# Performance work log

Hardware: AMD Instinct MI355X
Metric: run time of the kernel (lower is better)

## Reference

```python
import jax, jax.numpy as jnp
import numpy as np

D_MODEL = 1024
NUM_HEADS = 16
D_K = D_MODEL // NUM_HEADS
THETA = 10000.0
SEQ = 4096
BATCH = 1


def _rope(x, pos):
    # x: [..., S, d_k]; pos: [S]
    inv_freq = 1.0 / (THETA ** (jnp.arange(0, D_K, 2, dtype=jnp.float32) / D_K))  # [d_k/2]
    freqs = pos.astype(jnp.float32)[:, None] * inv_freq[None, :]  # [S, d_k/2]
    cos = jnp.cos(freqs)
    sin = jnp.sin(freqs)
    x_even = x[..., ::2]
    x_odd = x[..., 1::2]
    out1 = cos * x_even - sin * x_odd
    out2 = sin * x_even + cos * x_odd
    # interleave: stack on new last axis then flatten (matches torch.stack(...,-1).flatten(-2))
    out = jnp.stack([out1, out2], axis=-1).reshape(x.shape)
    return out


def setup_inputs() -> dict:
    key = jax.random.key(0)
    ks = jax.random.split(key, 5)
    std = (2.0 / (D_MODEL + D_MODEL)) ** 0.5
    x = jax.random.normal(ks[0], (BATCH, SEQ, D_MODEL), dtype=jnp.float32)
    wq = jax.random.normal(ks[1], (D_MODEL, D_MODEL), dtype=jnp.float32) * std
    wk = jax.random.normal(ks[2], (D_MODEL, D_MODEL), dtype=jnp.float32) * std
    wv = jax.random.normal(ks[3], (D_MODEL, D_MODEL), dtype=jnp.float32) * std
    wo = jax.random.normal(ks[4], (D_MODEL, D_MODEL), dtype=jnp.float32) * std
    return {"x": x, "wq": wq, "wk": wk, "wv": wv, "wo": wo}


def reference(x, wq, wk, wv, wo):
    b, s, d = x.shape
    # projections: y = x @ W.T  (weight stored [out, in])
    q = jnp.einsum('bsd,od->bso', x, wq)
    k = jnp.einsum('bsd,od->bso', x, wk)
    v = jnp.einsum('bsd,od->bso', x, wv)
    # split heads -> [b, h, s, d_k]
    q = q.reshape(b, s, NUM_HEADS, D_K).transpose(0, 2, 1, 3)
    k = k.reshape(b, s, NUM_HEADS, D_K).transpose(0, 2, 1, 3)
    v = v.reshape(b, s, NUM_HEADS, D_K).transpose(0, 2, 1, 3)
    pos = jnp.arange(s)
    q = _rope(q, pos)
    k = _rope(k, pos)
    scores = jnp.einsum('bhqd,bhkd->bhqk', q, k) / (D_K ** 0.5)
    causal = jnp.tril(jnp.ones((s, s), dtype=bool))
    scores = jnp.where(causal, scores, -jnp.inf)
    attn = jax.nn.softmax(scores, axis=-1)
    out = jnp.einsum('bhqk,bhkd->bhqd', attn, v)
    out = out.transpose(0, 2, 1, 3).reshape(b, s, d)
    out = jnp.einsum('bsd,od->bso', out, wo)
    return out
```

## Files before the change

kernel.cpp:

```cpp
#include <hip/hip_runtime.h>
#include <math.h>

#define SEQ    4096
#define DMODEL 1024
#define NHEADS 16
#define DK     64

typedef unsigned short u16;
typedef short bh8 __attribute__((ext_vector_type(8)));
typedef float f4  __attribute__((ext_vector_type(4)));
typedef float f16v __attribute__((ext_vector_type(16)));

__device__ __forceinline__ u16 f2b(float f) {
    union { float f; unsigned u; } v; v.f = f;
    unsigned u = v.u;
    return (u16)((u + 0x7FFFu + ((u >> 16) & 1u)) >> 16);
}
__device__ __forceinline__ unsigned pk2(float a, float b) {
    union { float f; unsigned u; } ua, ub; ua.f = a; ub.f = b;
    return (ua.u >> 16) | (ub.u & 0xFFFF0000u);
}

__global__ void cvt_all_kernel(const float* __restrict__ x,
                               const float* __restrict__ wq, const float* __restrict__ wk,
                               const float* __restrict__ wv, const float* __restrict__ wo,
                               u16* __restrict__ xb, u16* __restrict__ wb)
{
    const int NX = SEQ * DMODEL / 8;
    const int NW = DMODEL * DMODEL / 8;
    int i = blockIdx.x * blockDim.x + threadIdx.x;
    if (i >= NX + 4 * NW) return;
    const float* src; u16* dst; int j;
    if (i < NX) { src = x; dst = xb; j = i; }
    else {
        int k = i - NX;
        int wsel = k >> 17;
        j = k & (NW - 1);
        src = (wsel == 0) ? wq : (wsel == 1) ? wk : (wsel == 2) ? wv : wo;
        dst = wb + (size_t)wsel * DMODEL * DMODEL;
    }
    const float4* p = (const float4*)src + (size_t)j * 2;
    float4 a = p[0], b = p[1];
    __align__(16) u16 r[8] = { f2b(a.x), f2b(a.y), f2b(a.z), f2b(a.w),
                               f2b(b.x), f2b(b.y), f2b(b.z), f2b(b.w) };
    *(uint4*)(dst + (size_t)j * 8) = *(const uint4*)r;
}

template<int MODE>
__global__ __launch_bounds__(256) void gemm_bt(
    const u16* __restrict__ A, const u16* __restrict__ B,
    void* __restrict__ out, u16* __restrict__ Qh, u16* __restrict__ Kh,
    u16* __restrict__ Vt, int M, int N, int K)
{
    constexpr int BN = (MODE == 0) ? 64 : 128;
    constexpr int NJ = BN / 32;

    __shared__ __align__(16) u16 As[128 * 32];
    __shared__ __align__(16) u16 Bs[BN * 32];

    const int t    = threadIdx.x;
    const int w    = t >> 6, lane = t & 63;
    const int quad = lane >> 4, l16 = lane & 15;
    const int wm   = w >> 1,  wn  = w & 1;
    const int m0   = blockIdx.y * 128, n0 = blockIdx.x * BN;
    const int lr   = lane >> 2;
    const int lc   = (lane & 3) * 8;

    f4 acc[4][NJ];
#pragma unroll
    for (int i = 0; i < 4; ++i)
#pragma unroll
        for (int j = 0; j < NJ; ++j) { f4 z = {0.f,0.f,0.f,0.f}; acc[i][j] = z; }

    const int c0 = 2 * w, c1 = 2 * w + 1;

    for (int k0 = 0; k0 < K; k0 += 32) {
        __builtin_amdgcn_global_load_lds(
            (const __attribute__((address_space(1))) unsigned int*)(A + (size_t)(m0 + c0*16 + lr)*K + k0 + lc),
            (__attribute__((address_space(3))) unsigned int*)(As + c0*512), 16, 0, 0);
        __builtin_amdgcn_global_load_lds(
            (const __attribute__((address_space(1))) unsigned int*)(A + (size_t)(m0 + c1*16 + lr)*K + k0 + lc),
            (__attribute__((address_space(3))) unsigned int*)(As + c1*512), 16, 0, 0);
        if (MODE == 0) {
            __builtin_amdgcn_global_load_lds(
                (const __attribute__((address_space(1))) unsigned int*)(B + (size_t)(n0 + w*16 + lr)*K + k0 + lc),
                (__attribute__((address_space(3))) unsigned int*)(Bs + w*512), 16, 0, 0);
        } else {
            __builtin_amdgcn_global_load_lds(
                (const __attribute__((address_space(1))) unsigned int*)(B + (size_t)(n0 + c0*16 + lr)*K + k0 + lc),
                (__attribute__((address_space(3))) unsigned int*)(Bs + c0*512), 16, 0, 0);
            __builtin_amdgcn_global_load_lds(
                (const __attribute__((address_space(1))) unsigned int*)(B + (size_t)(n0 + c1*16 + lr)*K + k0 + lc),
                (__attribute__((address_space(3))) unsigned int*)(Bs + c1*512), 16, 0, 0);
        }
        __syncthreads();

        bh8 af[4], bf_[NJ];
#pragma unroll
        for (int i = 0; i < 4; ++i)
            af[i] = *(const bh8*)&As[(wm*64 + i*16 + l16)*32 + quad*8];
#pragma unroll
        for (int j = 0; j < NJ; ++j)
            bf_[j] = *(const bh8*)&Bs[(wn*(BN/2) + j*16 + l16)*32 + quad*8];
#pragma unroll
        for (int i = 0; i < 4; ++i)
#pragma unroll
            for (int j = 0; j < NJ; ++j)
                acc[i][j] = __builtin_amdgcn_mfma_f32_16x16x32_bf16(af[i], bf_[j], acc[i][j], 0, 0, 0);
        __syncthreads();
    }

    if (MODE == 0) {
#pragma unroll
        for (int i = 0; i < 4; ++i) {
            const int row = m0 + wm*64 + i*16 + quad*4;
#pragma unroll
            for (int j = 0; j < NJ; ++j) {
                const int col = n0 + wn*(BN/2) + j*16 + l16;
#pragma unroll
                for (int r = 0; r < 4; ++r)
                    ((float*)out)[(size_t)(row + r) * N + col] = acc[i][j][r];
            }
        }
    } else {
        const int sect  = n0 >> 10;
        const int cbase = (n0 & 1023) + wn * 64;
        const int hh    = cbase >> 6;
        if (sect < 2) {
            u16* dst = (sect == 0) ? Qh : Kh;
            const float qscl = (sect == 0) ? 0.18033688011112042f : 1.0f;
#pragma unroll
            for (int j = 0; j < NJ; ++j) {
                const int d = j * 16 + l16;
                const float invf2 = exp2f((float)(d & ~1) * (-13.287712379549449f / 64.0f))
                                    * 0.15915494309189535f;
#pragma unroll
                for (int i = 0; i < 4; ++i) {
                    const int srow0 = m0 + wm*64 + i*16 + quad*4;
#pragma unroll
                    for (int r = 0; r < 4; ++r) {
                        float own = acc[i][j][r];
                        float oth = __shfl_xor(own, 1);
                        float rev = (float)(srow0 + r) * invf2;
                        rev -= floorf(rev);
                        float sn = __builtin_amdgcn_sinf(rev);
                        float cs = __builtin_amdgcn_cosf(rev);
                        float xe = (l16 & 1) ? oth : own;
                        float xo = (l16 & 1) ? own : oth;
                        float val = (l16 & 1) ? (sn * xe + cs * xo)
                                              : (cs * xe - sn * xo);
                        dst[((size_t)hh * SEQ + srow0 + r) * DK + d] = f2b(val * qscl);
                    }
                }
            }
        } else {
#pragma unroll
            for (int j = 0; j < NJ; ++j) {
                const int d = j * 16 + l16;
#pragma unroll
                for (int i = 0; i < 4; ++i) {
                    const int srow0 = m0 + wm*64 + i*16 + quad*4;
                    __align__(8) u16 pk[4];
#pragma unroll
                    for (int r = 0; r < 4; ++r) pk[r] = f2b(acc[i][j][r]);
                    *(unsigned long long*)&Vt[((size_t)hh * DK + d) * SEQ + srow0] =
                        *(const unsigned long long*)pk;
                }
            }
        }
    }
}

__global__ __launch_bounds__(512, 4) void attn_mfma_kernel(
    const u16* __restrict__ Qh, const u16* __restrict__ Kh,
    const u16* __restrict__ Vt, u16* __restrict__ ctx)
{
    __shared__ __align__(16) u16 smem[2][16384];

    const int id   = blockIdx.x;
    const int head = (id & 7) + 8 * ((id >> 3) & 1);
    const int bx   = id >> 4;

    const int t    = threadIdx.x;
    const int w    = t >> 6, lane = t & 63;
    const int qb   = w & 1, kb = w >> 1;
    const int l31  = lane & 31, hl = lane >> 5;
    const int r7   = l31 & 7;

    const u16* Kbase = Kh + (size_t)head * SEQ * DK;
    const u16* Vbase = Vt + (size_t)head * DK * SEQ;

    int kread[4];
#pragma unroll
    for (int c = 0; c < 4; ++c)
        kread[c] = (kb * 32 + l31) * 64 + (((c * 2 + hl) ^ r7) * 8);
    int vread[2][2];
#pragma unroll
    for (int db = 0; db < 2; ++db)
#pragma unroll
        for (int kc = 0; kc < 2; ++kc)
            vread[db][kc] = (db * 32 + l31) * 128
                          + (((kb * 4 + kc * 2 + hl) ^ r7) * 8);

    int koff[2], voff[2];
#pragma unroll
    for (int i = 0; i < 2; ++i) {
        const int krow = i * 64 + (t >> 3);
        koff[i] = krow * DK + (((t & 7) ^ (krow & 7)) * 8);
        const int vdr  = i * 32 + (t >> 4);
        voff[i] = vdr * SEQ + (((t & 15) ^ (vdr & 7)) * 8);
    }
    const int dstK = w * 512;
    const int dstV = 8192 + w * 512;

#define STAGE(buf_, kbase_) do {                                               \
    _Pragma("unroll")                                                          \
    for (int i_ = 0; i_ < 2; ++i_) {                                           \
        __builtin_amdgcn_global_load_lds(                                      \
            (const __attribute__((address_space(1))) unsigned int*)            \
                (Kbase + (size_t)(kbase_) * DK + koff[i_]),                    \
            (__attribute__((address_space(3))) unsigned int*)                  \
                &smem[buf_][i_ * 4096 + dstK], 16, 0, 0);                      \
        __builtin_amdgcn_global_load_lds(                                      \
            (const __attribute__((address_space(1))) unsigned int*)            \
                (Vbase + (kbase_) + voff[i_]),                                 \
            (__attribute__((address_space(3))) unsigned int*)                  \
                &smem[buf_][i_ * 4096 + dstV], 16, 0, 0);                      \
    }                                                                          \
} while (0)

    for (int part = 0; part < 2; ++part) {
        const int qt = part ? (63 - bx) : bx;
        const int q0 = qt * 64;
        const int nt = qt / 2 + 1;
        const int qg = q0 + qb * 32 + l31;

        bh8 qa[4];
        {
            const u16* qrow = Qh + ((size_t)head * SEQ + qg) * DK;
#pragma unroll
            for (int c = 0; c < 4; ++c)
                qa[c] = *(const bh8*)(qrow + c * 16 + hl * 8);
        }

        f16v o0 = {0,0,0,0,0,0,0,0,0,0,0,0,0,0,0,0};
        f16v o1 = {0,0,0,0,0,0,0,0,0,0,0,0,0,0,0,0};
        float lsum = 0.f;

        __syncthreads();
        STAGE(0, 0);
        __syncthreads();

        int b = 0;
        for (int kt = 0; kt < nt; ++kt) {
            const bool have_next = (kt + 1 < nt);
            if (have_next) STAGE(b ^ 1, (kt + 1) * 128);

            const int  kbase = kt * 128;
            const bool diag  = (kt == nt - 1);
            const bool skip  = diag && (kbase + kb * 32 > q0 + qb * 32 + 31);

            if (!skip) {
                f16v s = {0,0,0,0,0,0,0,0,0,0,0,0,0,0,0,0};
                __builtin_amdgcn_s_setprio(1);
#pragma unroll
                for (int c = 0; c < 4; ++c) {
                    bh8 kf = *(const bh8*)&smem[b][kread[c]];
                    s = __builtin_amdgcn_mfma_f32_32x32x16_bf16(kf, qa[c], s, 0, 0, 0);
                }
                __builtin_amdgcn_s_setprio(0);
                if (diag) {
#pragma unroll
                    for (int r = 0; r < 16; ++r) {
                        const int keyg = kbase + kb * 32 + (r & 3) + 8 * (r >> 2) + 4 * hl;
                        if (keyg > qg) s[r] = -1.0e30f;
                    }
                }
                float p[16];
#pragma unroll
                for (int r = 0; r < 16; ++r) { p[r] = exp2f(s[r]); lsum += p[r]; }

#pragma unroll
                for (int kc = 0; kc < 2; ++kc) {
                    unsigned A0 = pk2(p[kc*8+0], p[kc*8+1]);
                    unsigned A1 = pk2(p[kc*8+2], p[kc*8+3]);
                    unsigned A2 = pk2(p[kc*8+4], p[kc*8+5]);
                    unsigned A3 = pk2(p[kc*8+6], p[kc*8+7]);
                    asm volatile("v_permlane32_swap_b32 %0, %1" : "+v"(A0), "+v"(A2));
                    asm volatile("v_permlane32_swap_b32 %0, %1" : "+v"(A1), "+v"(A3));
                    union { unsigned u[4]; bh8 v; } pb;
                    pb.u[0] = A0; pb.u[1] = A1; pb.u[2] = A2; pb.u[3] = A3;
                    bh8 va0 = *(const bh8*)&smem[b][8192 + vread[0][kc]];
                    bh8 va1 = *(const bh8*)&smem[b][8192 + vread[1][kc]];
                    __builtin_amdgcn_s_setprio(1);
                    o0 = __builtin_amdgcn_mfma_f32_32x32x16_bf16(va0, pb.v, o0, 0, 0, 0);
                    o1 = __builtin_amdgcn_mfma_f32_32x32x16_bf16(va1, pb.v, o1, 0, 0, 0);
                    __builtin_amdgcn_s_setprio(0);
                }
            }

            if (have_next) { __syncthreads(); b ^= 1; }
        }

        lsum += __shfl_xor(lsum, 32);
        __syncthreads();
        float* scr = (float*)&smem[0][0];
        union { f16v v; f4 q[4]; } uo0, uo1;
        uo0.v = o0; uo1.v = o1;
        if (kb != 0) {
            float* rec = scr + (((kb - 1) * 2 + qb) * 64 + lane) * 33;
#pragma unroll
            for (int j = 0; j < 4; ++j) {
                *(f4*)(rec + j * 4)      = uo0.q[j];
                *(f4*)(rec + 16 + j * 4) = uo1.q[j];
            }
            rec[32] = lsum;
        }
        __syncthreads();
        if (kb == 0) {
#pragma unroll
            for (int jr = 0; jr < 3; ++jr) {
                const float* rec = scr + ((jr * 2 + qb) * 64 + lane) * 33;
#pragma unroll
                for (int j = 0; j < 4; ++j) {
                    f4 a = *(const f4*)(rec + j * 4);
                    f4 c = *(const f4*)(rec + 16 + j * 4);
#pragma unroll
                    for (int e = 0; e < 4; ++e) {
                        uo0.q[j][e] += a[e];
                        uo1.q[j][e] += c[e];
                    }
                }
                lsum += rec[32];
            }
            const float linv = 1.f / lsum;
            const size_t rowbase = (size_t)qg * DMODEL + head * DK;
#pragma unroll
            for (int a = 0; a < 4; ++a) {
                unsigned lo = (unsigned)f2b(uo0.q[a][0] * linv) | ((unsigned)f2b(uo0.q[a][1] * linv) << 16);
                unsigned hi = (unsigned)f2b(uo0.q[a][2] * linv) | ((unsigned)f2b(uo0.q[a][3] * linv) << 16);
                uint2 pkd; pkd.x = lo; pkd.y = hi;
                *(uint2*)&ctx[rowbase + a * 8 + 4 * hl] = pkd;
                lo = (unsigned)f2b(uo1.q[a][0] * linv) | ((unsigned)f2b(uo1.q[a][1] * linv) << 16);
                hi = (unsigned)f2b(uo1.q[a][2] * linv) | ((unsigned)f2b(uo1.q[a][3] * linv) << 16);
                pkd.x = lo; pkd.y = hi;
                *(uint2*)&ctx[rowbase + 32 + a * 8 + 4 * hl] = pkd;
            }
        }
    }
#undef STAGE
}

extern "C" void kernel_launch(void* const* d_in, const int* in_sizes, int n_in,
                              void* d_out, int out_size, void* d_ws, size_t ws_size,
                              hipStream_t stream)
{
    const float* x  = (const float*)d_in[0];
    const float* wq = (const float*)d_in[1];
    const float* wk = (const float*)d_in[2];
    const float* wv = (const float*)d_in[3];
    const float* wo = (const float*)d_in[4];
    float* out = (float*)d_out;

    char* ws = (char*)d_ws;
    const size_t MB = 1u << 20;
    u16* xb   = (u16*)(ws);
    u16* wqkv = (u16*)(ws + 8  * MB);
    u16* wob  = (u16*)(ws + 14 * MB);
    u16* Qh   = (u16*)(ws + 16 * MB);
    u16* Kh   = (u16*)(ws + 24 * MB);
    u16* Vtb  = (u16*)(ws + 32 * MB);
    u16* ctxb = (u16*)(ws + 40 * MB);

    const int NCVT = SEQ * DMODEL / 8 + 4 * (DMODEL * DMODEL / 8);
    cvt_all_kernel<<<NCVT / 256, 256, 0, stream>>>(x, wq, wk, wv, wo, xb, wqkv);

    dim3 gqkv(3 * DMODEL / 128, SEQ / 128);
    gemm_bt<2><<<gqkv, 256, 0, stream>>>(xb, wqkv, nullptr, Qh, Kh, Vtb,
                                         SEQ, 3 * DMODEL, DMODEL);

    attn_mfma_kernel<<<dim3(512), 512, 0, stream>>>(Qh, Kh, Vtb, ctxb);

    dim3 go(DMODEL / 64, SEQ / 128);
    gemm_bt<0><<<go, 256, 0, stream>>>(ctxb, wob, out, nullptr, nullptr, nullptr,
                                       SEQ, DMODEL, DMODEL);
}
```

Measured before the change: 216.7 us.

## Double-buffer projection GEMM LDS and vectorize QKV epilogue stores

Double-buffers the shared-memory tiles in the bf16 projection GEMM so the next K-slice's global-to-LDS loads are issued before computing the current slice, removing one barrier per iteration. For the QKV mode, B rows are loaded in a permuted order so each lane holds four consecutive head dims, which lets the RoPE epilogue pair even and odd dims in registers without shuffles and store 8-byte packed vectors. The V transpose is staged through swizzled LDS so Vt is written with 16-byte coalesced stores. The cost is doubled LDS per block, which may reduce occupancy, plus more index arithmetic.

```diff
diff --git a/kernel.cpp b/kernel.cpp
--- a/kernel.cpp
+++ b/kernel.cpp
@@ -52,11 +52,12 @@
     void* __restrict__ out, u16* __restrict__ Qh, u16* __restrict__ Kh,
     u16* __restrict__ Vt, int M, int N, int K)
 {
-    constexpr int BN = (MODE == 0) ? 64 : 128;
-    constexpr int NJ = BN / 32;
-
-    __shared__ __align__(16) u16 As[128 * 32];
-    __shared__ __align__(16) u16 Bs[BN * 32];
+    constexpr int BN  = (MODE == 0) ? 64 : 128;
+    constexpr int NJ  = BN / 32;
+    constexpr int ASZ = 128 * 32;
+    constexpr int BSZ = BN * 32;
+
+    __shared__ __align__(16) u16 sh[2][ASZ + BSZ];
 
     const int t    = threadIdx.x;
     const int w    = t >> 6, lane = t & 63;
@@ -65,6 +66,7 @@
     const int m0   = blockIdx.y * 128, n0 = blockIdx.x * BN;
     const int lr   = lane >> 2;
     const int lc   = (lane & 3) * 8;
+    const int c0   = 2 * w, c1 = 2 * w + 1;
 
     f4 acc[4][NJ];
 #pragma unroll
@@ -72,103 +74,141 @@
 #pragma unroll
         for (int j = 0; j < NJ; ++j) { f4 z = {0.f,0.f,0.f,0.f}; acc[i][j] = z; }
 
-    const int c0 = 2 * w, c1 = 2 * w + 1;
-
+    const size_t aofs0 = (size_t)(m0 + c0 * 16 + lr) * K + lc;
+    const size_t aofs1 = (size_t)(m0 + c1 * 16 + lr) * K + lc;
+    size_t bofs0 = 0, bofs1 = 0;
+    if (MODE == 0) {
+        bofs0 = (size_t)(n0 + w * 16 + lr) * K + lc;
+    } else {
+        const int br0 = c0 * 16 + lr, br1 = c1 * 16 + lr;
+        const int p0 = (br0 & 64) | ((br0 & 15) << 2) | ((br0 >> 4) & 3);
+        const int p1 = (br1 & 64) | ((br1 & 15) << 2) | ((br1 >> 4) & 3);
+        bofs0 = (size_t)(n0 + p0) * K + lc;
+        bofs1 = (size_t)(n0 + p1) * K + lc;
+    }
+
+#define GLD(src_, dst_)                                                        \
+    __builtin_amdgcn_global_load_lds(                                          \
+        (const __attribute__((address_space(1))) unsigned int*)(src_),         \
+        (__attribute__((address_space(3))) unsigned int*)(dst_), 16, 0, 0)
+
+#define STAGE(buf_, k0_) do {                                                  \
+    GLD(A + aofs0 + (k0_), &sh[buf_][c0 * 512]);                               \
+    GLD(A + aofs1 + (k0_), &sh[buf_][c1 * 512]);                               \
+    if (MODE == 0) {                                                           \
+        GLD(B + bofs0 + (k0_), &sh[buf_][ASZ + w * 512]);                      \
+    } else {                                                                   \
+        GLD(B + bofs0 + (k0_), &sh[buf_][ASZ + c0 * 512]);                     \
+        GLD(B + bofs1 + (k0_), &sh[buf_][ASZ + c1 * 512]);                     \
+    }                                                                          \
+} while (0)
+
+    STAGE(0, 0);
+    __syncthreads();
+
+    int b = 0;
     for (int k0 = 0; k0 < K; k0 += 32) {
-        __builtin_amdgcn_global_load_lds(
-            (const __attribute__((address_space(1))) unsigned int*)(A + (size_t)(m0 + c0*16 + lr)*K + k0 + lc),
-            (__attribute__((address_space(3))) unsigned int*)(As + c0*512), 16, 0, 0);
-        __builtin_amdgcn_global_load_lds(
-            (const __attribute__((address_space(1))) unsigned int*)(A + (size_t)(m0 + c1*16 + lr)*K + k0 + lc),
-            (__attribute__((address_space(3))) unsigned int*)(As + c1*512), 16, 0, 0);
-        if (MODE == 0) {
-            __builtin_amdgcn_global_load_lds(
-                (const __attribute__((address_space(1))) unsigned int*)(B + (size_t)(n0 + w*16 + lr)*K + k0 + lc),
-                (__attribute__((address_space(3))) unsigned int*)(Bs + w*512), 16, 0, 0);
-        } else {
-            __builtin_amdgcn_global_load_lds(
-                (const __attribute__((address_space(1))) unsigned int*)(B + (size_t)(n0 + c0*16 + lr)*K + k0 + lc),
-                (__attribute__((address_space(3))) unsigned int*)(Bs + c0*512), 16, 0, 0);
-            __builtin_amdgcn_global_load_lds(
-                (const __attribute__((address_space(1))) unsigned int*)(B + (size_t)(n0 + c1*16 + lr)*K + k0 + lc),
-                (__attribute__((address_space(3))) unsigned int*)(Bs + c1*512), 16, 0, 0);
-        }
-        __syncthreads();
-
+        if (k0 + 32 < K) STAGE(b ^ 1, k0 + 32);
+
+        const u16* As_ = &sh[b][0];
+        const u16* Bs_ = &sh[b][ASZ];
         bh8 af[4], bf_[NJ];
 #pragma unroll
         for (int i = 0; i < 4; ++i)
-            af[i] = *(const bh8*)&As[(wm*64 + i*16 + l16)*32 + quad*8];
+            af[i] = *(const bh8*)&As_[(wm * 64 + i * 16 + l16) * 32 + quad * 8];
 #pragma unroll
         for (int j = 0; j < NJ; ++j)
-            bf_[j] = *(const bh8*)&Bs[(wn*(BN/2) + j*16 + l16)*32 + quad*8];
+            bf_[j] = *(const bh8*)&Bs_[(wn * (BN / 2) + j * 16 + l16) * 32 + quad * 8];
 #pragma unroll
         for (int i = 0; i < 4; ++i)
 #pragma unroll
             for (int j = 0; j < NJ; ++j)
                 acc[i][j] = __builtin_amdgcn_mfma_f32_16x16x32_bf16(af[i], bf_[j], acc[i][j], 0, 0, 0);
         __syncthreads();
+        b ^= 1;
     }
 
     if (MODE == 0) {
 #pragma unroll
         for (int i = 0; i < 4; ++i) {
-            const int row = m0 + wm*64 + i*16 + quad*4;
+            const int row = m0 + wm * 64 + i * 16 + quad * 4;
 #pragma unroll
             for (int j = 0; j < NJ; ++j) {
-                const int col = n0 + wn*(BN/2) + j*16 + l16;
+                const int col = n0 + wn * (BN / 2) + j * 16 + l16;
 #pragma unroll
                 for (int r = 0; r < 4; ++r)
                     ((float*)out)[(size_t)(row + r) * N + col] = acc[i][j][r];
             }
         }
     } else {
-        const int sect  = n0 >> 10;
-        const int cbase = (n0 & 1023) + wn * 64;
-        const int hh    = cbase >> 6;
+        const int sect = n0 >> 10;
         if (sect < 2) {
+            const int hh = ((n0 & 1023) + wn * 64) >> 6;
             u16* dst = (sect == 0) ? Qh : Kh;
             const float qscl = (sect == 0) ? 0.18033688011112042f : 1.0f;
-#pragma unroll
-            for (int j = 0; j < NJ; ++j) {
-                const int d = j * 16 + l16;
-                const float invf2 = exp2f((float)(d & ~1) * (-13.287712379549449f / 64.0f))
-                                    * 0.15915494309189535f;
-#pragma unroll
-                for (int i = 0; i < 4; ++i) {
-                    const int srow0 = m0 + wm*64 + i*16 + quad*4;
-#pragma unroll
-                    for (int r = 0; r < 4; ++r) {
-                        float own = acc[i][j][r];
-                        float oth = __shfl_xor(own, 1);
-                        float rev = (float)(srow0 + r) * invf2;
-                        rev -= floorf(rev);
-                        float sn = __builtin_amdgcn_sinf(rev);
-                        float cs = __builtin_amdgcn_cosf(rev);
-                        float xe = (l16 & 1) ? oth : own;
-                        float xo = (l16 & 1) ? own : oth;
-                        float val = (l16 & 1) ? (sn * xe + cs * xo)
-                                              : (cs * xe - sn * xo);
-                        dst[((size_t)hh * SEQ + srow0 + r) * DK + d] = f2b(val * qscl);
-                    }
+            const int dbase = l16 * 4;
+            const float invfA = exp2f((float)(dbase)     * (-13.287712379549449f / 64.0f))
+                                * 0.15915494309189535f;
+            const float invfB = exp2f((float)(dbase + 2) * (-13.287712379549449f / 64.0f))
+                                * 0.15915494309189535f;
+#pragma unroll
+            for (int i = 0; i < 4; ++i) {
+                const int srow0 = m0 + wm * 64 + i * 16 + quad * 4;
+#pragma unroll
+                for (int r = 0; r < 4; ++r) {
+                    const int srow = srow0 + r;
+                    float revA = (float)srow * invfA;  revA -= floorf(revA);
+                    float revB = (float)srow * invfB;  revB -= floorf(revB);
+                    const float snA = __builtin_amdgcn_sinf(revA);
+                    const float csA = __builtin_amdgcn_cosf(revA);
+                    const float snB = __builtin_amdgcn_sinf(revB);
+                    const float csB = __builtin_amdgcn_cosf(revB);
+                    const float e0 = acc[i][0][r], o0 = acc[i][1][r];
+                    const float e1 = acc[i][2][r], o1 = acc[i][3][r];
+                    const float v0 = (csA * e0 - snA * o0) * qscl;
+                    const float v1 = (snA * e0 + csA * o0) * qscl;
+                    const float v2 = (csB * e1 - snB * o1) * qscl;
+                    const float v3 = (snB * e1 + csB * o1) * qscl;
+                    uint2 st;
+                    st.x = (unsigned)f2b(v0) | ((unsigned)f2b(v1) << 16);
+                    st.y = (unsigned)f2b(v2) | ((unsigned)f2b(v3) << 16);
+                    *(uint2*)&dst[((size_t)hh * SEQ + srow) * DK + dbase] = st;
                 }
             }
         } else {
-#pragma unroll
-            for (int j = 0; j < NJ; ++j) {
-                const int d = j * 16 + l16;
-#pragma unroll
-                for (int i = 0; i < 4; ++i) {
-                    const int srow0 = m0 + wm*64 + i*16 + quad*4;
+            u16* scr = &sh[0][0];
+            const int cfb = wn * 64 + l16 * 4;
+            const int xv  = (l16 & 7) << 2;
+            __syncthreads();
+#pragma unroll
+            for (int i = 0; i < 4; ++i) {
+                const int s0 = wm * 64 + i * 16 + quad * 4;
+                const int s8 = s0 >> 2;
+#pragma unroll
+                for (int j = 0; j < NJ; ++j) {
                     __align__(8) u16 pk[4];
 #pragma unroll
                     for (int r = 0; r < 4; ++r) pk[r] = f2b(acc[i][j][r]);
-                    *(unsigned long long*)&Vt[((size_t)hh * DK + d) * SEQ + srow0] =
+                    *(unsigned long long*)&scr[(cfb + j) * 128 + (s8 ^ xv) * 4] =
                         *(const unsigned long long*)pk;
                 }
             }
-        }
-    }
+            __syncthreads();
+            const int hh0 = (n0 & 1023) >> 6;
+            const int sl  = t & 15;
+#pragma unroll
+            for (int jj = 0; jj < 8; ++jj) {
+                const int cfull = jj * 16 + (t >> 4);
+                const int hd    = hh0 + (cfull >> 6);
+                const int dd    = cfull & 63;
+                const int rxv   = ((cfull >> 2) & 7) << 2;
+                bh8 vv = *(const bh8*)&scr[cfull * 128 + ((sl * 2) ^ rxv) * 4];
+                *(bh8*)&Vt[((size_t)hd * DK + dd) * SEQ + m0 + sl * 8] = vv;
+            }
+        }
+    }
+#undef STAGE
+#undef GLD
 }
 
 __global__ __launch_bounds__(512, 4) void attn_mfma_kernel(
```

New measurement: 204.1 us. 5.8% less time.
